# Performance work log

Measured on AMD Instinct MI355X. Metric: run time of the kernel, lower is better.

## Reference

```python
import jax, jax.numpy as jnp
import numpy as np

QB = 127.0  # act_bits=8 -> 2**(8-1)-1
EPS = 1e-5


def _ste(x, q):
    # straight-through estimator: forward = q, backward = identity
    return x + jax.lax.stop_gradient(q - x)


def bitlinear(x, W, b):
    """BitNet-b1.58 linear: ternary weights (per-tensor mean-abs scale),
    8-bit per-token absmax activations, dequantized matmul + bias."""
    w_scale = jnp.clip(jnp.mean(jnp.abs(W)), EPS, None)
    Wq = _ste(W, jnp.clip(jnp.round(W / w_scale), -1.0, 1.0) * w_scale)  # ternary * scale
    x_scale = jnp.clip(jnp.max(jnp.abs(x), axis=-1, keepdims=True), EPS, None)
    xq = _ste(x, jnp.clip(jnp.round(x * (QB / x_scale)), -QB - 1.0, QB) * (x_scale / QB))
    # x: [B, N, d_in], W: [d_out, d_in] -> [B, N, d_out]
    return jnp.einsum('bnd,hd->bnh', xq, Wq) + b


def setup_inputs() -> dict:
    key = jax.random.key(0)
    k0, k1, k2 = jax.random.split(key, 3)
    B, N, D = 8, 4096, 1024
    H = int(D * 4.0)
    x = jax.random.normal(k0, (B, N, D), dtype=jnp.float32)
    W1 = jax.random.normal(k1, (H, D), dtype=jnp.float32) * 0.02
    b1 = jnp.zeros((H,), dtype=jnp.float32)
    W2 = jax.random.normal(k2, (D, H), dtype=jnp.float32) * 0.02
    b2 = jnp.zeros((D,), dtype=jnp.float32)
    return {"x": x, "W1": W1, "b1": b1, "W2": W2, "b2": b2}


def reference(x, W1, b1, W2, b2):
    h = bitlinear(x, W1, b1)                 # [B, N, H]
    h = jax.nn.gelu(h, approximate=False)    # torch nn.GELU default = exact erf
    # dropout with p=0.0 is identity
    return bitlinear(h, W2, b2)              # [B, N, D]
```

## Files before the change

kernel.cpp:

```cpp
#include <hip/hip_runtime.h>
#include <hip/hip_bf16.h>
#include <math.h>


typedef int int32x4 __attribute__((ext_vector_type(4)));

typedef const void __attribute__((address_space(1))) gv_t;
typedef void __attribute__((address_space(3))) lv_t;

__device__ __forceinline__ void gload_lds16(const signed char* g,
                                            signed char* l) {
  __builtin_amdgcn_global_load_lds((gv_t*)g, (lv_t*)l, 16, 0, 0);
}

__device__ __forceinline__ float gelu_erf(float v) {
  return 0.5f * v * (1.0f + erff(v * 0.70710678118654752440f));
}

__device__ __forceinline__ void store_gt(float* p, float v) { *p = v; }
__device__ __forceinline__ void store_gt(__hip_bfloat16* p, float v) {
  unsigned u = __float_as_uint(v);
  u += 0x7fffu + ((u >> 16) & 1u);
  *(unsigned short*)p = (unsigned short)(u >> 16);
}

__device__ __forceinline__ void load4v(const float* p, float v[4]) {
  const float4 t = *(const float4*)p;
  v[0] = t.x; v[1] = t.y; v[2] = t.z; v[3] = t.w;
}
__device__ __forceinline__ void load4v(const __hip_bfloat16* p, float v[4]) {
  const ushort4 t = *(const ushort4*)p;
  v[0] = __uint_as_float((unsigned)t.x << 16);
  v[1] = __uint_as_float((unsigned)t.y << 16);
  v[2] = __uint_as_float((unsigned)t.z << 16);
  v[3] = __uint_as_float((unsigned)t.w << 16);
}

__global__ __launch_bounds__(256) void absmean_partial(
    const float* __restrict__ W, double* __restrict__ part) {
  const int tid = threadIdx.x;
  const long base = (long)blockIdx.x * 8192;
  double s = 0.0;
#pragma unroll
  for (int c = 0; c < 8; ++c) {
    const float4 v = *(const float4*)&W[base + c * 1024 + tid * 4];
    s += (double)fabsf(v.x) + (double)fabsf(v.y) +
         (double)fabsf(v.z) + (double)fabsf(v.w);
  }
  __shared__ double sm[256];
  sm[tid] = s; __syncthreads();
  for (int off = 128; off; off >>= 1) {
    if (tid < off) sm[tid] += sm[tid + off];
    __syncthreads();
  }
  if (tid == 0) part[blockIdx.x] = sm[0];
}

__global__ __launch_bounds__(256) void absmean_final(
    const double* __restrict__ part, double* __restrict__ out, double n) {
  const int tid = threadIdx.x;
  __shared__ double sm[256];
  sm[tid] = part[tid] + part[tid + 256];
  __syncthreads();
  for (int off = 128; off; off >>= 1) {
    if (tid < off) sm[tid] += sm[tid + off];
    __syncthreads();
  }
  if (tid == 0) out[0] = fmax(sm[0] / n, 1e-5);
}

__global__ __launch_bounds__(256) void quant_w(
    const float* __restrict__ W, const double* __restrict__ wsP,
    signed char* __restrict__ Wq) {
  const double ws = *wsP;
  const long i = ((long)blockIdx.x * 256 + threadIdx.x) * 4;
  const float4 v = *(const float4*)&W[i];
  const float vv[4] = {v.x, v.y, v.z, v.w};
  int pack = 0;
#pragma unroll
  for (int q = 0; q < 4; ++q) {
    double r = rint((double)vv[q] / ws);
    r = fmin(fmax(r, -1.0), 1.0);
    pack |= (((int)r) & 0xff) << (8 * q);
  }
  *(int*)&Wq[i] = pack;
}

template <int L, bool GELU, typename GT>
__global__ __launch_bounds__(256) void quant_rows(
    const GT* __restrict__ X, signed char* __restrict__ Xq,
    float* __restrict__ dsc) {
  constexpr int CH = L / 1024;
  const long row = blockIdx.x;
  const int tid = threadIdx.x;
  const GT* xr = X + row * (long)L;
  float v[CH][4];
  float m = 0.f;
#pragma unroll
  for (int c = 0; c < CH; ++c) {
    load4v(xr + c * 1024 + tid * 4, v[c]);
#pragma unroll
    for (int q = 0; q < 4; ++q) {
      if (GELU) v[c][q] = gelu_erf(v[c][q]);
      m = fmaxf(m, fabsf(v[c][q]));
    }
  }
#pragma unroll
  for (int off = 32; off; off >>= 1) m = fmaxf(m, __shfl_down(m, off, 64));
  __shared__ float wmx[4];
  if ((tid & 63) == 0) wmx[tid >> 6] = m;
  __syncthreads();
  float ms = fmaxf(fmaxf(wmx[0], wmx[1]), fmaxf(wmx[2], wmx[3]));
  ms = fmaxf(ms, 1e-5f);
  const double inv = 127.0 / (double)ms;
#pragma unroll
  for (int c = 0; c < CH; ++c) {
    int pack = 0;
#pragma unroll
    for (int q = 0; q < 4; ++q) {
      double r = rint((double)v[c][q] * inv);
      r = fmin(fmax(r, -128.0), 127.0);
      pack |= (((int)r) & 0xff) << (8 * q);
    }
    *(int*)&Xq[row * (long)L + c * 1024 + tid * 4] = pack;
  }
  if (tid == 0) dsc[row] = (float)((double)ms / 127.0);
}

template <typename GT>
__global__ __launch_bounds__(512, 2) void gemm_i8_8ph(
    const signed char* __restrict__ A, const signed char* __restrict__ Bm,
    const float* __restrict__ dA, const double* __restrict__ wsB,
    const float* __restrict__ bias, GT* __restrict__ C,
    int K, int Ncol, int nx) {
  __shared__ signed char LDS[131072];
  const int tid = threadIdx.x;
  const int lane = tid & 63;
  const int wave = tid >> 6;
  const int wm = wave >> 2;
  const int wn = wave & 3;

  const int cpx = gridDim.x >> 3;
  const int wg = ((int)blockIdx.x & 7) * cpx + ((int)blockIdx.x >> 3);
  const long rowBase = (long)(wg / nx) * 256;
  const long colBase = (long)(wg % nx) * 256;
  const int NT = K >> 7;

  const int dd = wave * 1024 + lane * 16;
  const int srow = dd >> 7;
  const int scol = (dd & 127) ^ ((srow & 7) << 4);
  const long k64 = 64L * K;
  const signed char* sA0 = A + (rowBase + srow) * (long)K + scol;
  const signed char* sB0 = Bm + (colBase + srow) * (long)K + scol;

  auto STAGE_A = [&](int t) {
    const signed char* p = sA0 + ((long)t << 7);
    signed char* l = &LDS[((t & 1) << 15) + dd];
#pragma unroll
    for (int i = 0; i < 4; ++i) gload_lds16(p + i * k64, l + i * 8192);
  };
  auto STAGE_B = [&](int t) {
    const signed char* p = sB0 + ((long)t << 7);
    signed char* l = &LDS[65536 + ((t & 1) << 15) + dd];
#pragma unroll
    for (int i = 0; i < 4; ++i) gload_lds16(p + i * k64, l + i * 8192);
  };

  const int rl = lane & 15;
  const int col0 = (((lane >> 4) << 4)) ^ ((rl & 7) << 4);
  const int aRow = wm * 16384 + rl * 128;
  const int bRow = wn * 8192 + rl * 128;

  int32x4 acc[8][4] = {};

  STAGE_B(0); STAGE_A(0); STAGE_B(1);
  asm volatile("s_waitcnt vmcnt(4)" ::: "memory");
  __builtin_amdgcn_s_barrier();

  for (int t = 0; t < NT; ++t) {
    const signed char* At = &LDS[(t & 1) << 15];
    const signed char* Bt = &LDS[65536 + ((t & 1) << 15)];
    int32x4 af[4], bf[4];

    auto LDA = [&](int mih, int kc6) {
#pragma unroll
      for (int i = 0; i < 4; ++i)
        af[i] = *(const int32x4*)(At + aRow + (mih * 4 + i) * 2048 +
                                  (col0 ^ kc6));
    };
    auto LDB = [&](int kc6) {
#pragma unroll
      for (int nj = 0; nj < 4; ++nj)
        bf[nj] = *(const int32x4*)(Bt + bRow + nj * 2048 + (col0 ^ kc6));
    };
    auto MFMA16 = [&](int mih) {
#pragma unroll
      for (int i = 0; i < 4; ++i)
#pragma unroll
        for (int nj = 0; nj < 4; ++nj)
          acc[mih * 4 + i][nj] = __builtin_amdgcn_mfma_i32_16x16x64_i8(
              af[i], bf[nj], acc[mih * 4 + i][nj], 0, 0, 0);
    };

    LDB(0);
    LDA(0, 0);
    if (t + 1 < NT) STAGE_A(t + 1);
    __builtin_amdgcn_s_barrier();
    __builtin_amdgcn_s_setprio(1);
    MFMA16(0);
    __builtin_amdgcn_s_setprio(0);
    asm volatile("s_waitcnt lgkmcnt(0)" ::: "memory");
    __builtin_amdgcn_s_barrier();

    LDA(1, 0);
    __builtin_amdgcn_s_barrier();
    __builtin_amdgcn_s_setprio(1);
    MFMA16(1);
    __builtin_amdgcn_s_setprio(0);
    asm volatile("s_waitcnt lgkmcnt(0)" ::: "memory");
    __builtin_amdgcn_s_barrier();

    LDB(64);
    LDA(0, 64);
    __builtin_amdgcn_s_barrier();
    __builtin_amdgcn_s_setprio(1);
    MFMA16(0);
    __builtin_amdgcn_s_setprio(0);
    asm volatile("s_waitcnt lgkmcnt(0)" ::: "memory");
    __builtin_amdgcn_s_barrier();

    LDA(1, 64);
    if (t + 2 < NT) STAGE_B(t + 2);
    if (t < NT - 2) asm volatile("s_waitcnt vmcnt(4)" ::: "memory");
    else            asm volatile("s_waitcnt vmcnt(0)" ::: "memory");
    __builtin_amdgcn_s_barrier();
    __builtin_amdgcn_s_setprio(1);
    MFMA16(1);
    __builtin_amdgcn_s_setprio(0);
    asm volatile("s_waitcnt lgkmcnt(0)" ::: "memory");
    __builtin_amdgcn_s_barrier();
  }

  const double wsd = *wsB;
  const int rq = (lane >> 4) << 2;
  float bv[4];
#pragma unroll
  for (int nj = 0; nj < 4; ++nj)
    bv[nj] = bias[colBase + wn * 64 + nj * 16 + rl];
#pragma unroll
  for (int mi = 0; mi < 8; ++mi) {
#pragma unroll
    for (int r = 0; r < 4; ++r) {
      const long row = rowBase + wm * 128 + mi * 16 + rq + r;
      const float sc = (float)((double)dA[row] * wsd);
      GT* crow = C + row * (long)Ncol + colBase + wn * 64 + rl;
#pragma unroll
      for (int nj = 0; nj < 4; ++nj)
        store_gt(&crow[nj * 16], (float)acc[mi][nj][r] * sc + bv[nj]);
    }
  }
}

extern "C" void kernel_launch(void* const* d_in, const int* in_sizes, int n_in,
                              void* d_out, int out_size, void* d_ws,
                              size_t ws_size, hipStream_t stream) {
  const float* x  = (const float*)d_in[0];
  const float* W1 = (const float*)d_in[1];
  const float* b1 = (const float*)d_in[2];
  const float* W2 = (const float*)d_in[3];
  const float* b2 = (const float*)d_in[4];
  const int D = in_sizes[4];
  const int H = in_sizes[2];
  const long M = (long)in_sizes[0] / D;
  float* out = (float*)d_out;

  if (D != 1024 || H != 4096 || (M % 256) != 0) return;

  char* wsp = (char*)d_ws;
  size_t off = 0;
  auto alloc = [&](size_t bytes) {
    void* p = wsp + off;
    off = (off + bytes + 255) & ~(size_t)255;
    return p;
  };
  signed char* wq1 = (signed char*)alloc((size_t)H * D);
  signed char* wq2 = (signed char*)alloc((size_t)D * H);
  signed char* xq  = (signed char*)alloc((size_t)M * D);
  signed char* gq  = (signed char*)alloc((size_t)M * H);
  float* dx = (float*)alloc((size_t)M * 4);
  float* dg = (float*)alloc((size_t)M * 4);
  double* part = (double*)alloc(512 * 8);
  double* ws1 = (double*)alloc(8);
  double* ws2 = (double*)alloc(8);
  __hip_bfloat16* h = (__hip_bfloat16*)alloc((size_t)M * H * 2);
  if (off > ws_size) return;

  const long nW = (long)H * D;
  absmean_partial<<<nW / 8192, 256, 0, stream>>>(W1, part);
  absmean_final<<<1, 256, 0, stream>>>(part, ws1, (double)nW);
  absmean_partial<<<nW / 8192, 256, 0, stream>>>(W2, part);
  absmean_final<<<1, 256, 0, stream>>>(part, ws2, (double)nW);
  quant_w<<<nW / 1024, 256, 0, stream>>>(W1, ws1, wq1);
  quant_w<<<nW / 1024, 256, 0, stream>>>(W2, ws2, wq2);
  quant_rows<1024, false, float><<<M, 256, 0, stream>>>(x, xq, dx);

  const int g1 = (H / 256) * (int)(M / 256);
  const int g2 = (D / 256) * (int)(M / 256);
  gemm_i8_8ph<__hip_bfloat16><<<g1, 512, 0, stream>>>(
      xq, wq1, dx, ws1, b1, h, D, H, H / 256);
  quant_rows<4096, true, __hip_bfloat16><<<M, 256, 0, stream>>>(h, gq, dg);
  gemm_i8_8ph<float><<<g2, 512, 0, stream>>>(
      gq, wq2, dg, ws2, b2, out, H, D, D / 256);
}
```

Before: 462.3 us.

## Restructure int8 GEMM main loop with fewer barriers and vectorized epilogue

The per-K-tile schedule drops from eight barriers to two. A-tile prefetch is split into two halves interleaved with the MFMA phases, and the vmcnt wait moves to the top of the loop. MFMA operands are swapped so each lane's accumulator holds four consecutive columns, which lets the epilogue issue vector stores (float4 or ushort4) and load bias as float4. Fewer barriers mean less wave stalling but more risk of LDS read/write hazards between waves, since staging of the next tile into the other buffer now relies on a single mid-loop barrier.

```diff
diff --git a/kernel.cpp b/kernel.cpp
--- a/kernel.cpp
+++ b/kernel.cpp
@@ -17,11 +17,21 @@
   return 0.5f * v * (1.0f + erff(v * 0.70710678118654752440f));
 }
 
-__device__ __forceinline__ void store_gt(float* p, float v) { *p = v; }
-__device__ __forceinline__ void store_gt(__hip_bfloat16* p, float v) {
+__device__ __forceinline__ unsigned short bf16_rne(float v) {
   unsigned u = __float_as_uint(v);
   u += 0x7fffu + ((u >> 16) & 1u);
-  *(unsigned short*)p = (unsigned short)(u >> 16);
+  return (unsigned short)(u >> 16);
+}
+
+__device__ __forceinline__ void store4(float* p, const float o[4]) {
+  float4 t; t.x = o[0]; t.y = o[1]; t.z = o[2]; t.w = o[3];
+  *(float4*)p = t;
+}
+__device__ __forceinline__ void store4(__hip_bfloat16* p, const float o[4]) {
+  ushort4 t;
+  t.x = bf16_rne(o[0]); t.y = bf16_rne(o[1]);
+  t.z = bf16_rne(o[2]); t.w = bf16_rne(o[3]);
+  *(ushort4*)p = t;
 }
 
 __device__ __forceinline__ void load4v(const float* p, float v[4]) {
@@ -128,7 +138,7 @@
 }
 
 template <typename GT>
-__global__ __launch_bounds__(512, 2) void gemm_i8_8ph(
+__global__ __launch_bounds__(512, 2) void gemm_i8_ls(
     const signed char* __restrict__ A, const signed char* __restrict__ Bm,
     const float* __restrict__ dA, const double* __restrict__ wsB,
     const float* __restrict__ bias, GT* __restrict__ C,
@@ -146,20 +156,20 @@
   const long colBase = (long)(wg % nx) * 256;
   const int NT = K >> 7;
 
-  const int dd = wave * 1024 + lane * 16;
+  const int dd = tid << 4;
   const int srow = dd >> 7;
   const int scol = (dd & 127) ^ ((srow & 7) << 4);
   const long k64 = 64L * K;
   const signed char* sA0 = A + (rowBase + srow) * (long)K + scol;
   const signed char* sB0 = Bm + (colBase + srow) * (long)K + scol;
 
-  auto STAGE_A = [&](int t) {
-    const signed char* p = sA0 + ((long)t << 7);
-    signed char* l = &LDS[((t & 1) << 15) + dd];
-#pragma unroll
-    for (int i = 0; i < 4; ++i) gload_lds16(p + i * k64, l + i * 8192);
+  auto STAGE_A2 = [&](int t, int h) {
+    const signed char* p = sA0 + ((long)t << 7) + (2 * h) * k64;
+    signed char* l = &LDS[((t & 1) << 15) + dd + h * 16384];
+    gload_lds16(p, l);
+    gload_lds16(p + k64, l + 8192);
   };
-  auto STAGE_B = [&](int t) {
+  auto STAGE_B4 = [&](int t) {
     const signed char* p = sB0 + ((long)t << 7);
     signed char* l = &LDS[65536 + ((t & 1) << 15) + dd];
 #pragma unroll
@@ -173,11 +183,15 @@
 
   int32x4 acc[8][4] = {};
 
-  STAGE_B(0); STAGE_A(0); STAGE_B(1);
-  asm volatile("s_waitcnt vmcnt(4)" ::: "memory");
-  __builtin_amdgcn_s_barrier();
+  STAGE_B4(0);
+  STAGE_A2(0, 0); STAGE_A2(0, 1);
+  STAGE_B4(1);
 
   for (int t = 0; t < NT; ++t) {
+    if (t + 1 < NT) asm volatile("s_waitcnt vmcnt(4)" ::: "memory");
+    else            asm volatile("s_waitcnt vmcnt(0)" ::: "memory");
+    __builtin_amdgcn_s_barrier();
+
     const signed char* At = &LDS[(t & 1) << 15];
     const signed char* Bt = &LDS[65536 + ((t & 1) << 15)];
     int32x4 af[4], bf[4];
@@ -194,69 +208,55 @@
         bf[nj] = *(const int32x4*)(Bt + bRow + nj * 2048 + (col0 ^ kc6));
     };
     auto MFMA16 = [&](int mih) {
+      __builtin_amdgcn_s_setprio(1);
 #pragma unroll
       for (int i = 0; i < 4; ++i)
 #pragma unroll
         for (int nj = 0; nj < 4; ++nj)
           acc[mih * 4 + i][nj] = __builtin_amdgcn_mfma_i32_16x16x64_i8(
-              af[i], bf[nj], acc[mih * 4 + i][nj], 0, 0, 0);
+              bf[nj], af[i], acc[mih * 4 + i][nj], 0, 0, 0);
+      __builtin_amdgcn_s_setprio(0);
     };
 
     LDB(0);
     LDA(0, 0);
-    if (t + 1 < NT) STAGE_A(t + 1);
-    __builtin_amdgcn_s_barrier();
-    __builtin_amdgcn_s_setprio(1);
+    if (t + 1 < NT) STAGE_A2(t + 1, 0);
     MFMA16(0);
-    __builtin_amdgcn_s_setprio(0);
+    LDA(1, 0);
+    if (t + 1 < NT) STAGE_A2(t + 1, 1);
+    MFMA16(1);
+    LDB(64);
+    LDA(0, 64);
+    MFMA16(0);
     asm volatile("s_waitcnt lgkmcnt(0)" ::: "memory");
     __builtin_amdgcn_s_barrier();
-
-    LDA(1, 0);
-    __builtin_amdgcn_s_barrier();
-    __builtin_amdgcn_s_setprio(1);
+    LDA(1, 64);
+    if (t + 2 < NT) STAGE_B4(t + 2);
     MFMA16(1);
-    __builtin_amdgcn_s_setprio(0);
-    asm volatile("s_waitcnt lgkmcnt(0)" ::: "memory");
-    __builtin_amdgcn_s_barrier();
-
-    LDB(64);
-    LDA(0, 64);
-    __builtin_amdgcn_s_barrier();
-    __builtin_amdgcn_s_setprio(1);
-    MFMA16(0);
-    __builtin_amdgcn_s_setprio(0);
-    asm volatile("s_waitcnt lgkmcnt(0)" ::: "memory");
-    __builtin_amdgcn_s_barrier();
-
-    LDA(1, 64);
-    if (t + 2 < NT) STAGE_B(t + 2);
-    if (t < NT - 2) asm volatile("s_waitcnt vmcnt(4)" ::: "memory");
-    else            asm volatile("s_waitcnt vmcnt(0)" ::: "memory");
-    __builtin_amdgcn_s_barrier();
-    __builtin_amdgcn_s_setprio(1);
-    MFMA16(1);
-    __builtin_amdgcn_s_setprio(0);
-    asm volatile("s_waitcnt lgkmcnt(0)" ::: "memory");
-    __builtin_amdgcn_s_barrier();
   }
 
   const double wsd = *wsB;
-  const int rq = (lane >> 4) << 2;
-  float bv[4];
+  const int rq4 = (lane >> 4) << 2;
+  float sc[8];
+#pragma unroll
+  for (int mi = 0; mi < 8; ++mi)
+    sc[mi] = (float)((double)dA[rowBase + wm * 128 + mi * 16 + rl] * wsd);
+  float4 bv[4];
 #pragma unroll
   for (int nj = 0; nj < 4; ++nj)
-    bv[nj] = bias[colBase + wn * 64 + nj * 16 + rl];
+    bv[nj] = *(const float4*)&bias[colBase + wn * 64 + nj * 16 + rq4];
 #pragma unroll
   for (int mi = 0; mi < 8; ++mi) {
-#pragma unroll
-    for (int r = 0; r < 4; ++r) {
-      const long row = rowBase + wm * 128 + mi * 16 + rq + r;
-      const float sc = (float)((double)dA[row] * wsd);
-      GT* crow = C + row * (long)Ncol + colBase + wn * 64 + rl;
-#pragma unroll
-      for (int nj = 0; nj < 4; ++nj)
-        store_gt(&crow[nj * 16], (float)acc[mi][nj][r] * sc + bv[nj]);
+    const long row = rowBase + wm * 128 + mi * 16 + rl;
+    GT* crow = C + row * (long)Ncol + colBase + wn * 64 + rq4;
+#pragma unroll
+    for (int nj = 0; nj < 4; ++nj) {
+      float o[4];
+      o[0] = (float)acc[mi][nj][0] * sc[mi] + bv[nj].x;
+      o[1] = (float)acc[mi][nj][1] * sc[mi] + bv[nj].y;
+      o[2] = (float)acc[mi][nj][2] * sc[mi] + bv[nj].z;
+      o[3] = (float)acc[mi][nj][3] * sc[mi] + bv[nj].w;
+      store4(&crow[nj * 16], o);
     }
   }
 }
@@ -306,9 +306,9 @@
 
   const int g1 = (H / 256) * (int)(M / 256);
   const int g2 = (D / 256) * (int)(M / 256);
-  gemm_i8_8ph<__hip_bfloat16><<<g1, 512, 0, stream>>>(
+  gemm_i8_ls<__hip_bfloat16><<<g1, 512, 0, stream>>>(
       xq, wq1, dx, ws1, b1, h, D, H, H / 256);
   quant_rows<4096, true, __hip_bfloat16><<<M, 256, 0, stream>>>(h, gq, dg);
-  gemm_i8_8ph<float><<<g2, 512, 0, stream>>>(
+  gemm_i8_ls<float><<<g2, 512, 0, stream>>>(
       gq, wq2, dg, ws2, b2, out, H, D, D / 256);
 }
```

Result: no change. 467.7 us (+1.2%).

## Unroll int8 GEMM main loop by two tiles with fixed LDS buffers

Applied to the files above, without the earlier changes.

The main K loop of the int8 MFMA GEMM now handles two K-tiles per iteration, so each tile has a compile-time LDS buffer. Global-to-LDS staging for the next tile is spread across the sub-phases, and the explicit lgkmcnt(0) waits between phases are dropped in favour of a vmcnt(0) wait at each half-iteration boundary. The aim is to cut per-phase synchronisation overhead and index arithmetic. In exchange, tiles are prefetched only about half a pass ahead instead of further, so global load latency may be less well hidden. The loop also assumes an even number of K-tiles.

```diff
diff --git a/kernel.cpp b/kernel.cpp
--- a/kernel.cpp
+++ b/kernel.cpp
@@ -128,7 +128,7 @@
 }
 
 template <typename GT>
-__global__ __launch_bounds__(512, 2) void gemm_i8_8ph(
+__global__ __launch_bounds__(512, 2) void gemm_i8_m201(
     const signed char* __restrict__ A, const signed char* __restrict__ Bm,
     const float* __restrict__ dA, const double* __restrict__ wsB,
     const float* __restrict__ bias, GT* __restrict__ C,
@@ -145,8 +145,9 @@
   const long rowBase = (long)(wg / nx) * 256;
   const long colBase = (long)(wg % nx) * 256;
   const int NT = K >> 7;
-
-  const int dd = wave * 1024 + lane * 16;
+  const int NI = NT >> 1;
+
+  const int dd = tid << 4;
   const int srow = dd >> 7;
   const int scol = (dd & 127) ^ ((srow & 7) << 4);
   const long k64 = 64L * K;
@@ -172,72 +173,86 @@
   const int bRow = wn * 8192 + rl * 128;
 
   int32x4 acc[8][4] = {};
-
-  STAGE_B(0); STAGE_A(0); STAGE_B(1);
-  asm volatile("s_waitcnt vmcnt(4)" ::: "memory");
+  int32x4 af[4], bf[4];
+
+  auto LDA = [&](const signed char* At, int mih, int kc6) {
+#pragma unroll
+    for (int i = 0; i < 4; ++i)
+      af[i] = *(const int32x4*)(At + aRow + (mih * 4 + i) * 2048 +
+                                (col0 ^ kc6));
+  };
+  auto LDB = [&](const signed char* Bt, int kc6) {
+#pragma unroll
+    for (int nj = 0; nj < 4; ++nj)
+      bf[nj] = *(const int32x4*)(Bt + bRow + nj * 2048 + (col0 ^ kc6));
+  };
+  auto MFMA16 = [&](int mih) {
+    __builtin_amdgcn_s_setprio(1);
+#pragma unroll
+    for (int i = 0; i < 4; ++i)
+#pragma unroll
+      for (int nj = 0; nj < 4; ++nj)
+        acc[mih * 4 + i][nj] = __builtin_amdgcn_mfma_i32_16x16x64_i8(
+            af[i], bf[nj], acc[mih * 4 + i][nj], 0, 0, 0);
+    __builtin_amdgcn_s_setprio(0);
+  };
+
+  STAGE_A(0); STAGE_B(0);
+  STAGE_A(1); STAGE_B(1);
+  asm volatile("s_waitcnt vmcnt(8)" ::: "memory");
   __builtin_amdgcn_s_barrier();
 
-  for (int t = 0; t < NT; ++t) {
-    const signed char* At = &LDS[(t & 1) << 15];
-    const signed char* Bt = &LDS[65536 + ((t & 1) << 15)];
-    int32x4 af[4], bf[4];
-
-    auto LDA = [&](int mih, int kc6) {
-#pragma unroll
-      for (int i = 0; i < 4; ++i)
-        af[i] = *(const int32x4*)(At + aRow + (mih * 4 + i) * 2048 +
-                                  (col0 ^ kc6));
-    };
-    auto LDB = [&](int kc6) {
-#pragma unroll
-      for (int nj = 0; nj < 4; ++nj)
-        bf[nj] = *(const int32x4*)(Bt + bRow + nj * 2048 + (col0 ^ kc6));
-    };
-    auto MFMA16 = [&](int mih) {
-#pragma unroll
-      for (int i = 0; i < 4; ++i)
-#pragma unroll
-        for (int nj = 0; nj < 4; ++nj)
-          acc[mih * 4 + i][nj] = __builtin_amdgcn_mfma_i32_16x16x64_i8(
-              af[i], bf[nj], acc[mih * 4 + i][nj], 0, 0, 0);
-    };
-
-    LDB(0);
-    LDA(0, 0);
-    if (t + 1 < NT) STAGE_A(t + 1);
-    __builtin_amdgcn_s_barrier();
-    __builtin_amdgcn_s_setprio(1);
+  for (int it = 0; it < NI; ++it) {
+    const int t0 = 2 * it, t1 = 2 * it + 1;
+    const signed char* A0 = &LDS[(t0 & 1) << 15];
+    const signed char* B0 = &LDS[65536 + ((t0 & 1) << 15)];
+    const signed char* A1 = &LDS[(t1 & 1) << 15];
+    const signed char* B1 = &LDS[65536 + ((t1 & 1) << 15)];
+
+    LDB(B0, 0); LDA(A0, 0, 0);
+    if (it > 0) STAGE_A(t1);
+    __builtin_amdgcn_s_barrier();
     MFMA16(0);
-    __builtin_amdgcn_s_setprio(0);
-    asm volatile("s_waitcnt lgkmcnt(0)" ::: "memory");
-    __builtin_amdgcn_s_barrier();
-
-    LDA(1, 0);
-    __builtin_amdgcn_s_barrier();
-    __builtin_amdgcn_s_setprio(1);
+    __builtin_amdgcn_s_barrier();
+
+    LDA(A0, 1, 0);
+    if (it > 0) STAGE_B(t1);
+    __builtin_amdgcn_s_barrier();
     MFMA16(1);
-    __builtin_amdgcn_s_setprio(0);
-    asm volatile("s_waitcnt lgkmcnt(0)" ::: "memory");
-    __builtin_amdgcn_s_barrier();
-
-    LDB(64);
-    LDA(0, 64);
-    __builtin_amdgcn_s_barrier();
-    __builtin_amdgcn_s_setprio(1);
+    __builtin_amdgcn_s_barrier();
+
+    LDB(B0, 64); LDA(A0, 0, 64);
+    __builtin_amdgcn_s_barrier();
     MFMA16(0);
-    __builtin_amdgcn_s_setprio(0);
-    asm volatile("s_waitcnt lgkmcnt(0)" ::: "memory");
-    __builtin_amdgcn_s_barrier();
-
-    LDA(1, 64);
-    if (t + 2 < NT) STAGE_B(t + 2);
-    if (t < NT - 2) asm volatile("s_waitcnt vmcnt(4)" ::: "memory");
-    else            asm volatile("s_waitcnt vmcnt(0)" ::: "memory");
-    __builtin_amdgcn_s_barrier();
-    __builtin_amdgcn_s_setprio(1);
+    __builtin_amdgcn_s_barrier();
+
+    LDA(A0, 1, 64);
+    __builtin_amdgcn_s_barrier();
     MFMA16(1);
-    __builtin_amdgcn_s_setprio(0);
-    asm volatile("s_waitcnt lgkmcnt(0)" ::: "memory");
+    asm volatile("s_waitcnt vmcnt(0)" ::: "memory");
+    __builtin_amdgcn_s_barrier();
+
+    LDB(B1, 0); LDA(A1, 0, 0);
+    if (it + 1 < NI) STAGE_A(t0 + 2);
+    __builtin_amdgcn_s_barrier();
+    MFMA16(0);
+    __builtin_amdgcn_s_barrier();
+
+    LDA(A1, 1, 0);
+    if (it + 1 < NI) STAGE_B(t0 + 2);
+    __builtin_amdgcn_s_barrier();
+    MFMA16(1);
+    __builtin_amdgcn_s_barrier();
+
+    LDB(B1, 64); LDA(A1, 0, 64);
+    __builtin_amdgcn_s_barrier();
+    MFMA16(0);
+    __builtin_amdgcn_s_barrier();
+
+    LDA(A1, 1, 64);
+    __builtin_amdgcn_s_barrier();
+    MFMA16(1);
+    asm volatile("s_waitcnt vmcnt(0)" ::: "memory");
     __builtin_amdgcn_s_barrier();
   }
 
@@ -306,9 +321,9 @@
 
   const int g1 = (H / 256) * (int)(M / 256);
   const int g2 = (D / 256) * (int)(M / 256);
-  gemm_i8_8ph<__hip_bfloat16><<<g1, 512, 0, stream>>>(
+  gemm_i8_m201<__hip_bfloat16><<<g1, 512, 0, stream>>>(
       xq, wq1, dx, ws1, b1, h, D, H, H / 256);
   quant_rows<4096, true, __hip_bfloat16><<<M, 256, 0, stream>>>(h, gq, dg);
-  gemm_i8_8ph<float><<<g2, 512, 0, stream>>>(
+  gemm_i8_m201<float><<<g2, 512, 0, stream>>>(
       gq, wq2, dg, ws2, b2, out, H, D, D / 256);
 }
```

Result: no change. 466.4 us (+0.9%).

## Shrink int8 GEMM tiles to 128x128 with 256 threads and simpler pipeline

Applied to the files above, without the earlier changes.

The int8 GEMM moves from 256x256 tiles with 8 waves and an 8-phase interleaved schedule to 128x128 tiles with 4 waves and 64KB of LDS. Each K step now stages both A and B at once, double-buffered, loads every fragment up front and issues all MFMAs with fewer barriers. The aim is higher occupancy and more workgroups to balance across CUs. The cost is roughly double the global and LDS traffic per output element and less overlap between LDS reads and MFMA work.

```diff
diff --git a/kernel.cpp b/kernel.cpp
--- a/kernel.cpp
+++ b/kernel.cpp
@@ -128,115 +128,92 @@
 }
 
 template <typename GT>
-__global__ __launch_bounds__(512, 2) void gemm_i8_8ph(
+__global__ __launch_bounds__(256, 2) void gemm_i8_occ(
     const signed char* __restrict__ A, const signed char* __restrict__ Bm,
     const float* __restrict__ dA, const double* __restrict__ wsB,
     const float* __restrict__ bias, GT* __restrict__ C,
     int K, int Ncol, int nx) {
-  __shared__ signed char LDS[131072];
+  __shared__ signed char LDS[65536];
   const int tid = threadIdx.x;
   const int lane = tid & 63;
   const int wave = tid >> 6;
-  const int wm = wave >> 2;
-  const int wn = wave & 3;
+  const int wm = wave >> 1;
+  const int wn = wave & 1;
 
   const int cpx = gridDim.x >> 3;
   const int wg = ((int)blockIdx.x & 7) * cpx + ((int)blockIdx.x >> 3);
-  const long rowBase = (long)(wg / nx) * 256;
-  const long colBase = (long)(wg % nx) * 256;
+  const long rowBase = (long)(wg / nx) * 128;
+  const long colBase = (long)(wg % nx) * 128;
   const int NT = K >> 7;
 
-  const int dd = wave * 1024 + lane * 16;
+  const int dd = tid << 4;
   const int srow = dd >> 7;
   const int scol = (dd & 127) ^ ((srow & 7) << 4);
-  const long k64 = 64L * K;
+  const long k32 = 32L * K;
   const signed char* sA0 = A + (rowBase + srow) * (long)K + scol;
   const signed char* sB0 = Bm + (colBase + srow) * (long)K + scol;
 
-  auto STAGE_A = [&](int t) {
-    const signed char* p = sA0 + ((long)t << 7);
-    signed char* l = &LDS[((t & 1) << 15) + dd];
-#pragma unroll
-    for (int i = 0; i < 4; ++i) gload_lds16(p + i * k64, l + i * 8192);
-  };
-  auto STAGE_B = [&](int t) {
-    const signed char* p = sB0 + ((long)t << 7);
-    signed char* l = &LDS[65536 + ((t & 1) << 15) + dd];
-#pragma unroll
-    for (int i = 0; i < 4; ++i) gload_lds16(p + i * k64, l + i * 8192);
+  auto STAGE = [&](int t) {
+    const signed char* pa = sA0 + ((long)t << 7);
+    const signed char* pb = sB0 + ((long)t << 7);
+    signed char* la = &LDS[((t & 1) << 14) + dd];
+    signed char* lb = &LDS[32768 + ((t & 1) << 14) + dd];
+#pragma unroll
+    for (int i = 0; i < 4; ++i) gload_lds16(pa + i * k32, la + i * 4096);
+#pragma unroll
+    for (int i = 0; i < 4; ++i) gload_lds16(pb + i * k32, lb + i * 4096);
   };
 
   const int rl = lane & 15;
   const int col0 = (((lane >> 4) << 4)) ^ ((rl & 7) << 4);
-  const int aRow = wm * 16384 + rl * 128;
+  const int aRow = wm * 8192 + rl * 128;
   const int bRow = wn * 8192 + rl * 128;
 
-  int32x4 acc[8][4] = {};
-
-  STAGE_B(0); STAGE_A(0); STAGE_B(1);
-  asm volatile("s_waitcnt vmcnt(4)" ::: "memory");
-  __builtin_amdgcn_s_barrier();
+  int32x4 acc[4][4] = {};
+  int32x4 af0[4], bf0[4], af1[4], bf1[4];
+
+  STAGE(0);
 
   for (int t = 0; t < NT; ++t) {
-    const signed char* At = &LDS[(t & 1) << 15];
-    const signed char* Bt = &LDS[65536 + ((t & 1) << 15)];
-    int32x4 af[4], bf[4];
-
-    auto LDA = [&](int mih, int kc6) {
-#pragma unroll
-      for (int i = 0; i < 4; ++i)
-        af[i] = *(const int32x4*)(At + aRow + (mih * 4 + i) * 2048 +
-                                  (col0 ^ kc6));
-    };
-    auto LDB = [&](int kc6) {
-#pragma unroll
-      for (int nj = 0; nj < 4; ++nj)
-        bf[nj] = *(const int32x4*)(Bt + bRow + nj * 2048 + (col0 ^ kc6));
-    };
-    auto MFMA16 = [&](int mih) {
-#pragma unroll
-      for (int i = 0; i < 4; ++i)
-#pragma unroll
-        for (int nj = 0; nj < 4; ++nj)
-          acc[mih * 4 + i][nj] = __builtin_amdgcn_mfma_i32_16x16x64_i8(
-              af[i], bf[nj], acc[mih * 4 + i][nj], 0, 0, 0);
-    };
-
-    LDB(0);
-    LDA(0, 0);
-    if (t + 1 < NT) STAGE_A(t + 1);
+    const signed char* At = &LDS[(t & 1) << 14];
+    const signed char* Bt = &LDS[32768 + ((t & 1) << 14)];
+
+    if (t + 1 < NT) {
+      STAGE(t + 1);
+      asm volatile("s_waitcnt vmcnt(8)" ::: "memory");
+    } else {
+      asm volatile("s_waitcnt vmcnt(0)" ::: "memory");
+    }
     __builtin_amdgcn_s_barrier();
+
+#pragma unroll
+    for (int i = 0; i < 4; ++i)
+      af0[i] = *(const int32x4*)(At + aRow + i * 2048 + col0);
+#pragma unroll
+    for (int j = 0; j < 4; ++j)
+      bf0[j] = *(const int32x4*)(Bt + bRow + j * 2048 + col0);
+#pragma unroll
+    for (int i = 0; i < 4; ++i)
+      af1[i] = *(const int32x4*)(At + aRow + i * 2048 + (col0 ^ 64));
+#pragma unroll
+    for (int j = 0; j < 4; ++j)
+      bf1[j] = *(const int32x4*)(Bt + bRow + j * 2048 + (col0 ^ 64));
+
     __builtin_amdgcn_s_setprio(1);
-    MFMA16(0);
+#pragma unroll
+    for (int i = 0; i < 4; ++i)
+#pragma unroll
+      for (int j = 0; j < 4; ++j)
+        acc[i][j] = __builtin_amdgcn_mfma_i32_16x16x64_i8(
+            af0[i], bf0[j], acc[i][j], 0, 0, 0);
+#pragma unroll
+    for (int i = 0; i < 4; ++i)
+#pragma unroll
+      for (int j = 0; j < 4; ++j)
+        acc[i][j] = __builtin_amdgcn_mfma_i32_16x16x64_i8(
+            af1[i], bf1[j], acc[i][j], 0, 0, 0);
     __builtin_amdgcn_s_setprio(0);
-    asm volatile("s_waitcnt lgkmcnt(0)" ::: "memory");
-    __builtin_amdgcn_s_barrier();
-
-    LDA(1, 0);
-    __builtin_amdgcn_s_barrier();
-    __builtin_amdgcn_s_setprio(1);
-    MFMA16(1);
-    __builtin_amdgcn_s_setprio(0);
-    asm volatile("s_waitcnt lgkmcnt(0)" ::: "memory");
-    __builtin_amdgcn_s_barrier();
-
-    LDB(64);
-    LDA(0, 64);
-    __builtin_amdgcn_s_barrier();
-    __builtin_amdgcn_s_setprio(1);
-    MFMA16(0);
-    __builtin_amdgcn_s_setprio(0);
-    asm volatile("s_waitcnt lgkmcnt(0)" ::: "memory");
-    __builtin_amdgcn_s_barrier();
-
-    LDA(1, 64);
-    if (t + 2 < NT) STAGE_B(t + 2);
-    if (t < NT - 2) asm volatile("s_waitcnt vmcnt(4)" ::: "memory");
-    else            asm volatile("s_waitcnt vmcnt(0)" ::: "memory");
-    __builtin_amdgcn_s_barrier();
-    __builtin_amdgcn_s_setprio(1);
-    MFMA16(1);
-    __builtin_amdgcn_s_setprio(0);
+
     asm volatile("s_waitcnt lgkmcnt(0)" ::: "memory");
     __builtin_amdgcn_s_barrier();
   }
@@ -248,10 +225,10 @@
   for (int nj = 0; nj < 4; ++nj)
     bv[nj] = bias[colBase + wn * 64 + nj * 16 + rl];
 #pragma unroll
-  for (int mi = 0; mi < 8; ++mi) {
+  for (int mi = 0; mi < 4; ++mi) {
 #pragma unroll
     for (int r = 0; r < 4; ++r) {
-      const long row = rowBase + wm * 128 + mi * 16 + rq + r;
+      const long row = rowBase + wm * 64 + mi * 16 + rq + r;
       const float sc = (float)((double)dA[row] * wsd);
       GT* crow = C + row * (long)Ncol + colBase + wn * 64 + rl;
 #pragma unroll
@@ -274,7 +251,7 @@
   const long M = (long)in_sizes[0] / D;
   float* out = (float*)d_out;
 
-  if (D != 1024 || H != 4096 || (M % 256) != 0) return;
+  if (D != 1024 || H != 4096 || (M % 128) != 0) return;
 
   char* wsp = (char*)d_ws;
   size_t off = 0;
@@ -304,11 +281,11 @@
   quant_w<<<nW / 1024, 256, 0, stream>>>(W2, ws2, wq2);
   quant_rows<1024, false, float><<<M, 256, 0, stream>>>(x, xq, dx);
 
-  const int g1 = (H / 256) * (int)(M / 256);
-  const int g2 = (D / 256) * (int)(M / 256);
-  gemm_i8_8ph<__hip_bfloat16><<<g1, 512, 0, stream>>>(
-      xq, wq1, dx, ws1, b1, h, D, H, H / 256);
+  const int g1 = (int)(M / 128) * (H / 128);
+  const int g2 = (int)(M / 128) * (D / 128);
+  gemm_i8_occ<__hip_bfloat16><<<g1, 256, 0, stream>>>(
+      xq, wq1, dx, ws1, b1, h, D, H, H / 128);
   quant_rows<4096, true, __hip_bfloat16><<<M, 256, 0, stream>>>(h, gq, dg);
-  gemm_i8_8ph<float><<<g2, 512, 0, stream>>>(
-      gq, wq2, dg, ws2, b2, out, H, D, D / 256);
-}
+  gemm_i8_occ<float><<<g2, 256, 0, stream>>>(
+      gq, wq2, dg, ws2, b2, out, H, D, D / 128);
+}
```

New measurement: 516.4 us. 1.12x slower.
